# Kernel tuning notes

Measured on AMD Instinct MI355X. Metric: run time of the kernel, lower is better.

Reference implementation:

```python
import math
import jax, jax.numpy as jnp
import numpy as np

N_TOKENS = 16384
IN_FEATURES = 4096
N_EXPERTS = 64
TOP_K = 2
CAPACITY_FACTOR = 1.25
# get_capacity(n_tokens * top_k, n_experts, capacity_factor)
CAPACITY = math.ceil(N_TOKENS * TOP_K / N_EXPERTS * CAPACITY_FACTOR)  # 640


def setup_inputs() -> dict:
    key = jax.random.key(0)
    kx, kw = jax.random.split(key)
    x = jax.random.normal(kx, (N_TOKENS, IN_FEATURES), dtype=jnp.float32)
    W = jax.random.normal(kw, (N_EXPERTS, IN_FEATURES), dtype=jnp.float32) * (1.0 / math.sqrt(IN_FEATURES))
    return {"x": x, "W": W}


def reference(x, W):
    # gate: Linear(in_features, n_experts, bias=False)
    logits = jnp.einsum("nd,ed->ne", x, W)  # [N, E]
    n, e = logits.shape

    # pre_softmax=False path: topk over logits then softmax over the k scores
    scores, top_idx = jax.lax.top_k(logits, TOP_K)              # [N, K]
    probs = jax.nn.softmax(scores.astype(jnp.float32), axis=-1).astype(logits.dtype)

    rows = jnp.arange(n)[:, None]                               # [N, 1]
    # scatter probs / ones into dense [N, E] masks (topk indices per row are unique)
    top_k_masked_gates = jnp.zeros_like(logits).at[rows, top_idx].set(probs)
    top_k_mask = jnp.zeros_like(logits).at[rows, top_idx].set(1.0)

    # capacity top-k along the token dim (dim=0) -> per-expert token selection
    _, cap_idx = jax.lax.top_k(top_k_masked_gates.T, CAPACITY)  # [E, CAP] token ids
    cap_mask = jnp.zeros_like(logits).at[cap_idx, jnp.arange(e)[:, None]].set(1.0)

    # pad_to_capacity=False branch
    final_mask = jnp.logical_and(top_k_mask > 0, cap_mask > 0)  # [N, E]
    drop_mask = jnp.logical_not(final_mask)
    exceed_mask = jnp.take_along_axis(drop_mask, top_idx, axis=1)  # [N, K]
    final_probs = probs * jnp.logical_not(exceed_mask)
    final_indices = jnp.where(exceed_mask, jnp.iinfo(jnp.int32).max, top_idx)
    tokens_per_expert_before_capacity = top_k_mask.sum(0)       # [E]

    return final_probs, final_indices, tokens_per_expert_before_capacity
```

## Files before the change

kernel.cpp:

```cpp
#include <hip/hip_runtime.h>
#include <math.h>

#define N_TOK  16384
#define DIM    4096
#define NE     64
#define CAP    640
#define KC     32
#define TM     128
#define NTILES (N_TOK / TM)


__device__ __forceinline__ void gl_lds16(const float* g, float* l) {
  __builtin_amdgcn_global_load_lds((const __attribute__((address_space(1))) void*)g,
                                   (__attribute__((address_space(3))) void*)l, 16, 0, 0);
}

__global__ __launch_bounds__(256, 3) void gemm_logits_kernel(
    const float* __restrict__ x, const float* __restrict__ W,
    float* __restrict__ partials, int ks) {
  const int tile  = blockIdx.x % NTILES;
  const int split = blockIdx.x / NTILES;
  const int klen  = DIM / ks;
  const int k0    = split * klen;
  const int t_base = tile * TM;

  __shared__ float xs[2][KC * TM];
  __shared__ float wss[2][KC * NE];

  const int tid = threadIdx.x;
  const int tg  = tid >> 3;
  const int eg  = tid & 7;
  const int lk  = tid & 7;

  const int klx  = 4 * (lk ^ ((tg >> 2) & 7));
  const int klw0 = 4 * (lk ^ (tg >> 3));
  const int klw1 = 4 * (lk ^ ((tg >> 3) + 4));

  const float* xg  = x + (size_t)(t_base + tg) * DIM + k0 + klx;
  const float* wg0 = W + (size_t)tg * DIM + k0 + klw0;
  const float* wg1 = W + (size_t)(tg + 32) * DIM + k0 + klw1;
  float* xl = &xs[0][0]  + tid * 4;
  float* wl = &wss[0][0] + tid * 4;

  float acc[4][8];
#pragma unroll
  for (int i = 0; i < 4; ++i)
#pragma unroll
    for (int j = 0; j < 8; ++j) acc[i][j] = 0.f;

  const int niter = klen / KC;

  {
    gl_lds16(xg,            xl);
    gl_lds16(xg + 32 * DIM, xl + 1024);
    gl_lds16(xg + 64 * DIM, xl + 2048);
    gl_lds16(xg + 96 * DIM, xl + 3072);
    gl_lds16(wg0, wl);
    gl_lds16(wg1, wl + 1024);
  }
  __syncthreads();

  const int twz = tg & 7;
  for (int it = 0; it < niter; ++it) {
    const int cur = it & 1;
    const int nxt = cur ^ 1;

    if (it + 1 < niter) {
      const int ko = (it + 1) * KC;
      gl_lds16(xg + ko,            xl + nxt * 4096);
      gl_lds16(xg + ko + 32 * DIM, xl + nxt * 4096 + 1024);
      gl_lds16(xg + ko + 64 * DIM, xl + nxt * 4096 + 2048);
      gl_lds16(xg + ko + 96 * DIM, xl + nxt * 4096 + 3072);
      gl_lds16(wg0 + ko, wl + nxt * 2048);
      gl_lds16(wg1 + ko, wl + nxt * 2048 + 1024);
    }

    const float* xb = &xs[cur][0];
    const float* wb = &wss[cur][0];
#pragma unroll
    for (int kq = 0; kq < 8; ++kq) {
      const int xo = 4 * (kq ^ twz);
      const int wo = 4 * (kq ^ eg);
      float xa[16];
#pragma unroll
      for (int i = 0; i < 4; ++i) {
        const float4 v = *(const float4*)(xb + (4 * tg + i) * 32 + xo);
        xa[i * 4 + 0] = v.x; xa[i * 4 + 1] = v.y; xa[i * 4 + 2] = v.z; xa[i * 4 + 3] = v.w;
      }
      float wa[32];
#pragma unroll
      for (int j = 0; j < 8; ++j) {
        const float4 v = *(const float4*)(wb + (8 * eg + j) * 32 + wo);
        wa[j * 4 + 0] = v.x; wa[j * 4 + 1] = v.y; wa[j * 4 + 2] = v.z; wa[j * 4 + 3] = v.w;
      }
#pragma unroll
      for (int i = 0; i < 4; ++i)
#pragma unroll
        for (int j = 0; j < 8; ++j) {
          acc[i][j] = fmaf(xa[i * 4 + 0], wa[j * 4 + 0], acc[i][j]);
          acc[i][j] = fmaf(xa[i * 4 + 1], wa[j * 4 + 1], acc[i][j]);
          acc[i][j] = fmaf(xa[i * 4 + 2], wa[j * 4 + 2], acc[i][j]);
          acc[i][j] = fmaf(xa[i * 4 + 3], wa[j * 4 + 3], acc[i][j]);
        }
    }

    __syncthreads();
  }

  float* outp = partials + (size_t)split * N_TOK * NE;
#pragma unroll
  for (int i = 0; i < 4; ++i) {
    const int t = t_base + tg * 4 + i;
    const float4 v0 = make_float4(acc[i][0], acc[i][1], acc[i][2], acc[i][3]);
    const float4 v1 = make_float4(acc[i][4], acc[i][5], acc[i][6], acc[i][7]);
    *(float4*)(outp + (size_t)t * NE + eg * 8)     = v0;
    *(float4*)(outp + (size_t)t * NE + eg * 8 + 4) = v1;
  }
}

__global__ __launch_bounds__(64) void route_kernel(
    const float* __restrict__ partials, int ks,
    float* __restrict__ out, int* __restrict__ ws_idx,
    float* __restrict__ ws_probs, int* __restrict__ counts) {
  __shared__ int cnt[NE];
  const int tid = threadIdx.x;
  cnt[tid] = 0;
  __syncthreads();
  const int t = blockIdx.x * 64 + tid;

  float4 s[16];
  {
    const float* p = partials + (size_t)t * NE;
#pragma unroll
    for (int c = 0; c < 16; ++c) s[c] = *(const float4*)(p + 4 * c);
  }
  for (int sp = 1; sp < ks; ++sp) {
    const float* p = partials + (size_t)sp * N_TOK * NE + (size_t)t * NE;
#pragma unroll
    for (int c = 0; c < 16; ++c) {
      const float4 v = *(const float4*)(p + 4 * c);
      s[c].x += v.x; s[c].y += v.y; s[c].z += v.z; s[c].w += v.w;
    }
  }

  float b1 = -INFINITY, b2 = -INFINITY;
  int i1 = 0, i2 = 0;
#pragma unroll
  for (int c = 0; c < 16; ++c) {
    const float vv[4] = {s[c].x, s[c].y, s[c].z, s[c].w};
#pragma unroll
    for (int j = 0; j < 4; ++j) {
      const float v = vv[j];
      const int idx = c * 4 + j;
      if (v > b1)      { b2 = b1; i2 = i1; b1 = v; i1 = idx; }
      else if (v > b2) { b2 = v; i2 = idx; }
    }
  }
  const float ed = expf(b2 - b1);
  const float p1 = 1.0f / (1.0f + ed);
  const float p2 = ed / (1.0f + ed);

  out[(size_t)t * 2]     = p1;
  out[(size_t)t * 2 + 1] = p2;
  out[(size_t)N_TOK * 2 + t * 2]     = (float)i1;
  out[(size_t)N_TOK * 2 + t * 2 + 1] = (float)i2;
  ws_idx[t * 2] = i1;  ws_idx[t * 2 + 1] = i2;
  ws_probs[t * 2] = p1; ws_probs[t * 2 + 1] = p2;

  atomicAdd(&cnt[i1], 1);
  atomicAdd(&cnt[i2], 1);
  __syncthreads();
  atomicAdd(&counts[tid], cnt[tid]);
}

__global__ __launch_bounds__(256) void capacity_kernel(
    const int* __restrict__ counts, const int* __restrict__ ws_idx,
    const float* __restrict__ ws_probs, float* __restrict__ out) {
  const int e = blockIdx.x;
  const int cnt = counts[e];
  if (threadIdx.x == 0) out[(size_t)N_TOK * 4 + e] = (float)cnt;
  if (cnt <= CAP) return;
  for (int i = threadIdx.x; i < N_TOK * 2; i += 256) {
    if (ws_idx[i] != e) continue;
    const float p = ws_probs[i];
    const int tok = i >> 1;
    int rank = 0;
    for (int j = 0; j < N_TOK * 2; ++j) {
      if (ws_idx[j] != e) continue;
      const float q = ws_probs[j];
      if (q > p || (q == p && (j >> 1) < tok)) ++rank;
    }
    if (rank >= CAP) {
      out[i] = 0.0f;
      out[(size_t)N_TOK * 2 + i] = 2147483648.0f;
    }
  }
}

extern "C" void kernel_launch(void* const* d_in, const int* in_sizes, int n_in,
                              void* d_out, int out_size, void* d_ws, size_t ws_size,
                              hipStream_t stream) {
  const float* x = (const float*)d_in[0];
  const float* W = (const float*)d_in[1];
  float* out = (float*)d_out;

  char* ws = (char*)d_ws;
  int*   counts   = (int*)ws;
  int*   ws_idx   = (int*)(ws + 256);
  float* ws_probs = (float*)(ws + 256 + (size_t)N_TOK * 2 * 4);
  float* partials = (float*)(ws + 262400);

  const size_t base = 262400;
  const size_t per  = (size_t)N_TOK * NE * 4;
  int ks = 1;
  if (ws_size >= base + 8 * per)      ks = 8;
  else if (ws_size >= base + 4 * per) ks = 4;
  else if (ws_size >= base + 2 * per) ks = 2;

  hipMemsetAsync(counts, 0, NE * sizeof(int), stream);
  gemm_logits_kernel<<<NTILES * ks, 256, 0, stream>>>(x, W, partials, ks);
  route_kernel<<<N_TOK / 64, 64, 0, stream>>>(partials, ks, out, ws_idx, ws_probs, counts);
  capacity_kernel<<<NE, 256, 0, stream>>>(counts, ws_idx, ws_probs, out);
}
```

Baseline: 443.1 us.

## Transpose W once and read wave-uniform weights via scalar loads in GEMM

A new kernel transposes W into a k-major workspace buffer so each wave reads a contiguous 16-expert slice per k. Those reads are wave-uniform and can go through scalar loads instead of LDS. The GEMM tiling changes so each thread owns two tokens and 16 experts, and the W tile is no longer staged in shared memory, which frees LDS and LDS bandwidth. The cost is an extra launch, a workspace region for Wt, fewer tokens per accumulator row, and occupancy lowered to 2 blocks per CU in launch bounds.

```diff
diff --git a/kernel.cpp b/kernel.cpp
--- a/kernel.cpp
+++ b/kernel.cpp
@@ -15,8 +15,15 @@
                                    (__attribute__((address_space(3))) void*)l, 16, 0, 0);
 }
 
-__global__ __launch_bounds__(256, 3) void gemm_logits_kernel(
-    const float* __restrict__ x, const float* __restrict__ W,
+__global__ __launch_bounds__(256) void wt_kernel(
+    const float* __restrict__ W, float* __restrict__ Wt) {
+  const int idx = blockIdx.x * 256 + threadIdx.x;
+  const int k = idx >> 6, e = idx & 63;
+  Wt[idx] = W[(size_t)e * DIM + k];
+}
+
+__global__ __launch_bounds__(256, 2) void gemm_logits_kernel(
+    const float* __restrict__ x, const float* __restrict__ Wt,
     float* __restrict__ partials, int ks) {
   const int tile  = blockIdx.x % NTILES;
   const int split = blockIdx.x / NTILES;
@@ -25,42 +32,32 @@
   const int t_base = tile * TM;
 
   __shared__ float xs[2][KC * TM];
-  __shared__ float wss[2][KC * NE];
-
-  const int tid = threadIdx.x;
-  const int tg  = tid >> 3;
-  const int eg  = tid & 7;
-  const int lk  = tid & 7;
-
-  const int klx  = 4 * (lk ^ ((tg >> 2) & 7));
-  const int klw0 = 4 * (lk ^ (tg >> 3));
-  const int klw1 = 4 * (lk ^ ((tg >> 3) + 4));
-
-  const float* xg  = x + (size_t)(t_base + tg) * DIM + k0 + klx;
-  const float* wg0 = W + (size_t)tg * DIM + k0 + klw0;
-  const float* wg1 = W + (size_t)(tg + 32) * DIM + k0 + klw1;
-  float* xl = &xs[0][0]  + tid * 4;
-  float* wl = &wss[0][0] + tid * 4;
-
-  float acc[4][8];
-#pragma unroll
-  for (int i = 0; i < 4; ++i)
-#pragma unroll
-    for (int j = 0; j < 8; ++j) acc[i][j] = 0.f;
+
+  const int tid  = threadIdx.x;
+  const int tg   = tid >> 3;
+  const int lk   = tid & 7;
+  const int lane = tid & 63;
+  const int lkey = lane & 7;
+  const int wv   = __builtin_amdgcn_readfirstlane(tid >> 6);
+
+  const int klx = 4 * (lk ^ (tg & 7));
+  const float* xg = x + (size_t)(t_base + tg) * DIM + k0 + klx;
+  float* xl = &xs[0][0] + tid * 4;
+
+  const float* wtw = Wt + (size_t)k0 * NE + wv * 16;
+
+  float acc0[16], acc1[16];
+#pragma unroll
+  for (int e = 0; e < 16; ++e) { acc0[e] = 0.f; acc1[e] = 0.f; }
 
   const int niter = klen / KC;
 
-  {
-    gl_lds16(xg,            xl);
-    gl_lds16(xg + 32 * DIM, xl + 1024);
-    gl_lds16(xg + 64 * DIM, xl + 2048);
-    gl_lds16(xg + 96 * DIM, xl + 3072);
-    gl_lds16(wg0, wl);
-    gl_lds16(wg1, wl + 1024);
-  }
+  gl_lds16(xg,            xl);
+  gl_lds16(xg + 32 * DIM, xl + 1024);
+  gl_lds16(xg + 64 * DIM, xl + 2048);
+  gl_lds16(xg + 96 * DIM, xl + 3072);
   __syncthreads();
 
-  const int twz = tg & 7;
   for (int it = 0; it < niter; ++it) {
     const int cur = it & 1;
     const int nxt = cur ^ 1;
@@ -71,50 +68,41 @@
       gl_lds16(xg + ko + 32 * DIM, xl + nxt * 4096 + 1024);
       gl_lds16(xg + ko + 64 * DIM, xl + nxt * 4096 + 2048);
       gl_lds16(xg + ko + 96 * DIM, xl + nxt * 4096 + 3072);
-      gl_lds16(wg0 + ko, wl + nxt * 2048);
-      gl_lds16(wg1 + ko, wl + nxt * 2048 + 1024);
-    }
-
-    const float* xb = &xs[cur][0];
-    const float* wb = &wss[cur][0];
+    }
+
+    const float* xb  = &xs[cur][0];
+    const float* wtt = wtw + (size_t)it * KC * NE;
 #pragma unroll
     for (int kq = 0; kq < 8; ++kq) {
-      const int xo = 4 * (kq ^ twz);
-      const int wo = 4 * (kq ^ eg);
-      float xa[16];
-#pragma unroll
-      for (int i = 0; i < 4; ++i) {
-        const float4 v = *(const float4*)(xb + (4 * tg + i) * 32 + xo);
-        xa[i * 4 + 0] = v.x; xa[i * 4 + 1] = v.y; xa[i * 4 + 2] = v.z; xa[i * 4 + 3] = v.w;
+      const int xo = 4 * (kq ^ lkey);
+      const float4 xa0 = *(const float4*)(xb + lane * 32 + xo);
+      const float4 xa1 = *(const float4*)(xb + (lane + 64) * 32 + xo);
+      const float x0[4] = {xa0.x, xa0.y, xa0.z, xa0.w};
+      const float x1[4] = {xa1.x, xa1.y, xa1.z, xa1.w};
+#pragma unroll
+      for (int j = 0; j < 4; ++j) {
+        const float* wk = wtt + (kq * 4 + j) * NE;
+#pragma unroll
+        for (int e = 0; e < 16; ++e) {
+          const float w = wk[e];
+          acc0[e] = fmaf(x0[j], w, acc0[e]);
+          acc1[e] = fmaf(x1[j], w, acc1[e]);
+        }
       }
-      float wa[32];
-#pragma unroll
-      for (int j = 0; j < 8; ++j) {
-        const float4 v = *(const float4*)(wb + (8 * eg + j) * 32 + wo);
-        wa[j * 4 + 0] = v.x; wa[j * 4 + 1] = v.y; wa[j * 4 + 2] = v.z; wa[j * 4 + 3] = v.w;
-      }
-#pragma unroll
-      for (int i = 0; i < 4; ++i)
-#pragma unroll
-        for (int j = 0; j < 8; ++j) {
-          acc[i][j] = fmaf(xa[i * 4 + 0], wa[j * 4 + 0], acc[i][j]);
-          acc[i][j] = fmaf(xa[i * 4 + 1], wa[j * 4 + 1], acc[i][j]);
-          acc[i][j] = fmaf(xa[i * 4 + 2], wa[j * 4 + 2], acc[i][j]);
-          acc[i][j] = fmaf(xa[i * 4 + 3], wa[j * 4 + 3], acc[i][j]);
-        }
     }
 
     __syncthreads();
   }
 
   float* outp = partials + (size_t)split * N_TOK * NE;
-#pragma unroll
-  for (int i = 0; i < 4; ++i) {
-    const int t = t_base + tg * 4 + i;
-    const float4 v0 = make_float4(acc[i][0], acc[i][1], acc[i][2], acc[i][3]);
-    const float4 v1 = make_float4(acc[i][4], acc[i][5], acc[i][6], acc[i][7]);
-    *(float4*)(outp + (size_t)t * NE + eg * 8)     = v0;
-    *(float4*)(outp + (size_t)t * NE + eg * 8 + 4) = v1;
+  const int t0 = t_base + lane;
+  const int t1 = t0 + 64;
+#pragma unroll
+  for (int q = 0; q < 4; ++q) {
+    *(float4*)(outp + (size_t)t0 * NE + wv * 16 + 4 * q) =
+        make_float4(acc0[4 * q], acc0[4 * q + 1], acc0[4 * q + 2], acc0[4 * q + 3]);
+    *(float4*)(outp + (size_t)t1 * NE + wv * 16 + 4 * q) =
+        make_float4(acc1[4 * q], acc1[4 * q + 1], acc1[4 * q + 2], acc1[4 * q + 3]);
   }
 }
 
@@ -208,9 +196,10 @@
   int*   counts   = (int*)ws;
   int*   ws_idx   = (int*)(ws + 256);
   float* ws_probs = (float*)(ws + 256 + (size_t)N_TOK * 2 * 4);
-  float* partials = (float*)(ws + 262400);
-
-  const size_t base = 262400;
+  float* Wt       = (float*)(ws + 262400);
+  float* partials = (float*)(ws + 262400 + (size_t)DIM * NE * 4);
+
+  const size_t base = 262400 + (size_t)DIM * NE * 4;
   const size_t per  = (size_t)N_TOK * NE * 4;
   int ks = 1;
   if (ws_size >= base + 8 * per)      ks = 8;
@@ -218,7 +207,8 @@
   else if (ws_size >= base + 2 * per) ks = 2;
 
   hipMemsetAsync(counts, 0, NE * sizeof(int), stream);
-  gemm_logits_kernel<<<NTILES * ks, 256, 0, stream>>>(x, W, partials, ks);
+  wt_kernel<<<DIM * NE / 256, 256, 0, stream>>>(W, Wt);
+  gemm_logits_kernel<<<NTILES * ks, 256, 0, stream>>>(x, Wt, partials, ks);
   route_kernel<<<N_TOK / 64, 64, 0, stream>>>(partials, ks, out, ws_idx, ws_probs, counts);
   capacity_kernel<<<NE, 256, 0, stream>>>(counts, ws_idx, ws_probs, out);
 }
```

Result: no change. 437.1 us (-1.4%).
